# Kernel tuning notes

Measured on AMD Instinct MI355X. Metric: run time of the kernel, lower is better.

Reference implementation:

```python
import jax, jax.numpy as jnp
import numpy as np

ALPHA = 1.702  # GLU sigmoid scale
LIMIT = 7.0    # clamp limit
B, S, H, E, F, TOP_K = 2, 1024, 768, 16, 768, 4


def setup_inputs() -> dict:
    key = jax.random.key(0)
    ks = jax.random.split(key, 7)
    return {
        "hidden_states": jax.random.normal(ks[0], (B, S, H), jnp.float32),
        "router_weight": jax.random.normal(ks[1], (E, H), jnp.float32) * 0.02,
        "router_bias": jax.random.normal(ks[2], (E,), jnp.float32) * 0.02,
        "gate_up_proj": jax.random.normal(ks[3], (E, H, 2 * F), jnp.float32) * 0.02,
        "gate_up_proj_bias": jax.random.normal(ks[4], (E, 2 * F), jnp.float32) * 0.02,
        "down_proj": jax.random.normal(ks[5], (E, F, H), jnp.float32) * 0.02,
        "down_proj_bias": jax.random.normal(ks[6], (E, H), jnp.float32) * 0.02,
        "top_k": TOP_K,
    }


def reference(hidden_states, router_weight, router_bias, gate_up_proj,
              gate_up_proj_bias, down_proj, down_proj_bias, top_k):
    b, s, h = hidden_states.shape
    x = hidden_states.reshape(-1, h)                      # [T, H]
    t = x.shape[0]
    # ---- TopK router ----
    logits = x @ router_weight.T + router_bias            # [T, E]
    top_val, top_idx = jax.lax.top_k(logits, top_k)       # [T, K]
    top_val = jax.nn.softmax(top_val, axis=-1)
    router_scores = jnp.zeros_like(logits).at[
        jnp.arange(t)[:, None], top_idx].set(top_val)     # [T, E]
    # ---- Dense (all-expert) FFN, as in the reference repeat+bmm ----
    gate_up = jnp.einsum('th,ehf->etf', x, gate_up_proj) \
        + gate_up_proj_bias[:, None, :]                   # [E, T, 2F]
    gate = jnp.minimum(gate_up[..., 0::2], LIMIT)         # clamp(max=limit)
    up = jnp.clip(gate_up[..., 1::2], -LIMIT, LIMIT)
    glu = gate * jax.nn.sigmoid(gate * ALPHA)
    expert_out = jnp.einsum('etf,efh->eth', (up + 1.0) * glu, down_proj) \
        + down_proj_bias[:, None, :]                      # [E, T, H]
    expert_out = expert_out.reshape(-1, b, s, h)          # [E, B, S, H]
    w = router_scores.T.reshape(-1, b, s)[..., None]      # [E, B, S, 1]
    routed_out = (expert_out * w).sum(axis=0)             # [B, S, H]
    return routed_out, router_scores
```

## Files before the change

kernel.cpp:

```cpp
#include <hip/hip_runtime.h>
#include <hip/hip_bf16.h>

#define T_TOK 2048
#define H_DIM 768
#define E_NUM 16
#define F_DIM 768
#define TWOF 1536
#define TOPK 4
#define NASSIGN 8192
#define BM 128
#define BK 64
#define KT 12
#define NTILE 80
#define NSLOTP (NTILE * BM)
#define MAXT1 10
#define CHUNK (BM * BK)
#define WTILE (64 * BK)
#define NRTR 256

typedef __bf16 bf16x8 __attribute__((ext_vector_type(8)));
typedef unsigned short us8 __attribute__((ext_vector_type(8)));
typedef float f32x4 __attribute__((ext_vector_type(4)));

__device__ __forceinline__ unsigned short f2bf(float f) {
  unsigned u = __float_as_uint(f);
  u += 0x7FFF + ((u >> 16) & 1);
  return (unsigned short)(u >> 16);
}

__device__ __forceinline__ void gl_lds16(const unsigned short* g, unsigned short* l) {
  __builtin_amdgcn_global_load_lds(
      (const __attribute__((address_space(1))) unsigned int*)g,
      (__attribute__((address_space(3))) unsigned int*)l, 16, 0, 0);
}

__global__ __launch_bounds__(256)
void router_kernel(const float* __restrict__ x, const float* __restrict__ rw,
                   const float* __restrict__ rb, float* __restrict__ scores,
                   int* __restrict__ tk_idx, float* __restrict__ tk_w,
                   int* __restrict__ tmap, float* __restrict__ wgrp) {
  __shared__ float lg[8][16], sc[8][16];
  const int bid = blockIdx.x;
  const int tid = threadIdx.x;
  const int t0 = bid * 8;
  if (tid < 40) {
    tmap[bid * 40 + tid] = 0;
    wgrp[bid * 40 + tid] = 0.0f;
  }
  const int lane32 = tid & 31, tok = tid >> 5;
  const int e = lane32 & 15, q2 = lane32 >> 4;
  const int t = t0 + tok;
  const float* xr = x + (size_t)t * H_DIM + q2 * 384;
  const float* wr = rw + (size_t)e * H_DIM + q2 * 384;
  double a0 = 0, a1 = 0, a2 = 0, a3 = 0;
  #pragma unroll 4
  for (int h = 0; h < 384; h += 4) {
    const f32x4 xv = *(const f32x4*)(xr + h);
    const f32x4 wv = *(const f32x4*)(wr + h);
    a0 += (double)xv[0] * (double)wv[0];
    a1 += (double)xv[1] * (double)wv[1];
    a2 += (double)xv[2] * (double)wv[2];
    a3 += (double)xv[3] * (double)wv[3];
  }
  double acc = (a0 + a1) + (a2 + a3);
  acc += __shfl_xor(acc, 16, 64);
  if (q2 == 0) lg[tok][e] = (float)acc + rb[e];
  __syncthreads();
  if (lane32 == 0) {
    float v[16];
    #pragma unroll
    for (int i = 0; i < 16; ++i) { v[i] = lg[tok][i]; sc[tok][i] = 0.0f; }
    int idx[TOPK]; float val[TOPK];
    for (int k = 0; k < TOPK; ++k) {
      float best = -3.4e38f; int bi = 0;
      for (int i = 0; i < 16; ++i)
        if (v[i] > best) { best = v[i]; bi = i; }
      idx[k] = bi; val[k] = best; v[bi] = -3.4e38f;
    }
    float s = 0.0f, ev[TOPK];
    for (int k = 0; k < TOPK; ++k) { ev[k] = expf(val[k] - val[0]); s += ev[k]; }
    for (int k = 0; k < TOPK; ++k) {
      float wgt = ev[k] / s;
      sc[tok][idx[k]] = wgt;
      tk_idx[t * TOPK + k] = idx[k];
      tk_w[t * TOPK + k] = wgt;
    }
  }
  __syncthreads();
  if (tid < 128)
    scores[(size_t)(t0 + (tid >> 4)) * 16 + (tid & 15)] = sc[tid >> 4][tid & 15];
}

__global__ __launch_bounds__(256)
void group_kernel(const int* __restrict__ tk_idx, const float* __restrict__ tk_w,
                  int* __restrict__ counts, int* __restrict__ offs,
                  int* __restrict__ tmap, float* __restrict__ wgrp) {
  __shared__ int hist[256][16];
  __shared__ int seg[16][16];
  __shared__ int cnt[16], eoff[16];
  const int tid = threadIdx.x;
  int loc[16];
  #pragma unroll
  for (int e = 0; e < 16; ++e) loc[e] = 0;
  const int base = tid * 32;
  int eid[32];
  for (int i = 0; i < 32; ++i) { int e = tk_idx[base + i]; eid[i] = e; loc[e]++; }
  #pragma unroll
  for (int e = 0; e < 16; ++e) hist[tid][e] = loc[e];
  __syncthreads();
  const int s = tid >> 4, e16 = tid & 15;
  {
    int sum = 0;
    #pragma unroll
    for (int j = 0; j < 16; ++j) sum += hist[s * 16 + j][e16];
    seg[s][e16] = sum;
  }
  __syncthreads();
  if (tid < 16) {
    int run = 0;
    #pragma unroll
    for (int s2 = 0; s2 < 16; ++s2) { int t = seg[s2][tid]; seg[s2][tid] = run; run += t; }
    cnt[tid] = run;
  }
  __syncthreads();
  {
    int run = seg[s][e16];
    #pragma unroll
    for (int j = 0; j < 16; ++j) { int t = hist[s * 16 + j][e16]; hist[s * 16 + j][e16] = run; run += t; }
  }
  __syncthreads();
  if (tid == 0) {
    int acc = 0;
    for (int e = 0; e < 16; ++e) { eoff[e] = acc; acc += (cnt[e] + BM - 1) / BM * BM; }
  }
  __syncthreads();
  if (tid < 16) { counts[tid] = cnt[tid]; offs[tid] = eoff[tid]; }
  int run[16];
  #pragma unroll
  for (int e = 0; e < 16; ++e) run[e] = hist[tid][e];
  for (int i = 0; i < 32; ++i) {
    int e = eid[i];
    int slot = eoff[e] + run[e]++;
    tmap[slot] = base + i;
    wgrp[slot] = tk_w[base + i];
  }
}

__global__ __launch_bounds__(512)
void convert_w_kernel(const float* __restrict__ gup, const float* __restrict__ dwn,
                      unsigned short* __restrict__ gw, unsigned short* __restrict__ uw,
                      unsigned short* __restrict__ dw) {
  const int ft = blockIdx.x, kt = blockIdx.y, z = blockIdx.z;
  const int tid = threadIdx.x;
  const int n = tid & 63, k8 = tid >> 6;
  const int doff = n * BK + 8 * (k8 ^ (n & 7));
  __shared__ unsigned short tg[WTILE], tu[WTILE];
  if (z < 16) {
    const int e = z;
    const float* src = gup + ((size_t)(e * H_DIM + kt * 64 + k8 * 8)) * TWOF
                           + 2 * (ft * 64 + n);
    us8 g, u;
    #pragma unroll
    for (int j = 0; j < 8; ++j) {
      const float2 p = *(const float2*)(src + (size_t)j * TWOF);
      g[j] = f2bf(p.x); u[j] = f2bf(p.y);
    }
    *(us8*)&tg[doff] = g;
    *(us8*)&tu[doff] = u;
    __syncthreads();
    const size_t tb = (((size_t)e * KT + kt) * 12 + ft) * WTILE;
    *(us8*)&gw[tb + tid * 8] = *(const us8*)&tg[tid * 8];
    *(us8*)&uw[tb + tid * 8] = *(const us8*)&tu[tid * 8];
  } else {
    const int e = z - 16;
    const float* src = dwn + ((size_t)(e * F_DIM + kt * 64 + k8 * 8)) * H_DIM
                           + ft * 64 + n;
    us8 o;
    #pragma unroll
    for (int j = 0; j < 8; ++j) o[j] = f2bf(src[(size_t)j * H_DIM]);
    *(us8*)&tg[doff] = o;
    __syncthreads();
    const size_t tb = (((size_t)e * KT + kt) * 12 + ft) * WTILE;
    *(us8*)&dw[tb + tid * 8] = *(const us8*)&tg[tid * 8];
  }
}

__global__ __launch_bounds__(256)
void convert_x_kernel(const float* __restrict__ x, const int* __restrict__ tmap,
                      unsigned short* __restrict__ xg) {
  const int tile = blockIdx.x;
  const int kt = blockIdx.y;
  const int tid = threadIdx.x;
  const int r = tid >> 1;
  const int c0 = (tid & 1) * 32;
  const int tok = tmap[tile * BM + r] >> 2;
  const float* src = x + (size_t)tok * H_DIM + kt * 64 + c0;
  unsigned short* dst = xg + ((size_t)tile * KT + kt) * CHUNK + r * BK;
  #pragma unroll
  for (int qq = 0; qq < 4; ++qq) {
    f32x4 a = *(const f32x4*)(src + 8 * qq);
    f32x4 b = *(const f32x4*)(src + 8 * qq + 4);
    us8 o;
    #pragma unroll
    for (int j = 0; j < 4; ++j) { o[j] = f2bf(a[j]); o[4+j] = f2bf(b[j]); }
    const int k8 = (c0 >> 3) + qq;
    *(us8*)&dst[8 * (k8 ^ (r & 7))] = o;
  }
}

__global__ __launch_bounds__(512)
void gemm1_kernel(const unsigned short* __restrict__ xg, const unsigned short* __restrict__ gw,
                  const unsigned short* __restrict__ uw, const float* __restrict__ gupb,
                  const int* __restrict__ counts, const int* __restrict__ offs,
                  unsigned short* __restrict__ act) {
  const int bid = blockIdx.x;
  const int swz = (bid & 7) * 120 + (bid >> 3);
  const int ey = swz / 6, ft = swz % 6;
  const int e = ey / MAXT1, tile = ey % MAXT1;
  const int count = counts[e];
  if (tile * BM >= count) return;
  const int tileg = (offs[e] >> 7) + tile;
  const int tid = threadIdx.x;
  const int wv = tid >> 6, lane = tid & 63;
  const int ml = lane & 15, lh = lane >> 4;
  const int wm = wv >> 2, wn = wv & 3;

  __shared__ unsigned short lA[CHUNK];
  __shared__ unsigned short lBg[CHUNK];
  __shared__ unsigned short lBu[CHUNK];

  const unsigned short* ab = xg + (size_t)tileg * KT * CHUNK;
  const unsigned short* gb = gw + ((size_t)e * KT * 12 + ft * 2) * WTILE;
  const unsigned short* ub = uw + ((size_t)e * KT * 12 + ft * 2) * WTILE;

  f32x4 accg[4][2] = {};
  f32x4 accu[4][2] = {};

  for (int kt = 0; kt < KT; ++kt) {
    const unsigned short* as = ab + kt * CHUNK;
    const unsigned short* gs = gb + (size_t)kt * 12 * WTILE;
    const unsigned short* us = ub + (size_t)kt * 12 * WTILE;
    gl_lds16(as + tid * 8, &lA[tid * 8]);
    gl_lds16(as + (512 + tid) * 8, &lA[(512 + tid) * 8]);
    gl_lds16(gs + tid * 8, &lBg[tid * 8]);
    gl_lds16(gs + (512 + tid) * 8, &lBg[(512 + tid) * 8]);
    gl_lds16(us + tid * 8, &lBu[tid * 8]);
    gl_lds16(us + (512 + tid) * 8, &lBu[(512 + tid) * 8]);
    __syncthreads();
    #pragma unroll
    for (int ks = 0; ks < 2; ++ks) {
      const int slot = ks * 4 + lh;
      bf16x8 af[4];
      #pragma unroll
      for (int mf = 0; mf < 4; ++mf) {
        const int ar = wm * 64 + mf * 16 + ml;
        af[mf] = __builtin_bit_cast(bf16x8, *(const us8*)&lA[ar * BK + 8 * (slot ^ (ar & 7))]);
      }
      #pragma unroll
      for (int nf = 0; nf < 2; ++nf) {
        const int br = wn * 32 + nf * 16 + ml;
        const int ba = (br >> 6) * WTILE + (br & 63) * BK + 8 * (slot ^ (br & 7));
        bf16x8 bg = __builtin_bit_cast(bf16x8, *(const us8*)&lBg[ba]);
        bf16x8 bu = __builtin_bit_cast(bf16x8, *(const us8*)&lBu[ba]);
        #pragma unroll
        for (int mf = 0; mf < 4; ++mf) {
          accg[mf][nf] = __builtin_amdgcn_mfma_f32_16x16x32_bf16(af[mf], bg, accg[mf][nf], 0, 0, 0);
          accu[mf][nf] = __builtin_amdgcn_mfma_f32_16x16x32_bf16(af[mf], bu, accu[mf][nf], 0, 0, 0);
        }
      }
    }
    __syncthreads();
  }
  unsigned short* tbuf = (wn & 2) ? lBg : lA;
  #pragma unroll
  for (int mf = 0; mf < 4; ++mf) {
    #pragma unroll
    for (int nf = 0; nf < 2; ++nf) {
      const int fcl = wn * 32 + nf * 16 + ml;
      const int c = fcl & 63;
      const int fc = ft * 128 + fcl;
      const float bgv = gupb[(size_t)e * TWOF + 2 * fc];
      const float buv = gupb[(size_t)e * TWOF + 2 * fc + 1];
      #pragma unroll
      for (int r = 0; r < 4; ++r) {
        const int m = wm * 64 + mf * 16 + lh * 4 + r;
        float g = accg[mf][nf][r] + bgv;
        float u = accu[mf][nf][r] + buv;
        g = fminf(g, 7.0f);
        u = fminf(fmaxf(u, -7.0f), 7.0f);
        const float glu = g / (1.0f + expf(-1.702f * g));
        tbuf[m * BK + 8 * ((c >> 3) ^ (m & 7)) + (c & 7)] = f2bf((u + 1.0f) * glu);
      }
    }
  }
  __syncthreads();
  unsigned short* ob0 = act + ((size_t)tileg * KT + ft * 2) * CHUNK;
  unsigned short* ob1 = ob0 + CHUNK;
  #pragma unroll
  for (int i = 0; i < 2; ++i) {
    *(us8*)&ob0[(i * 512 + tid) * 8] = *(const us8*)&lA[(i * 512 + tid) * 8];
    *(us8*)&ob1[(i * 512 + tid) * 8] = *(const us8*)&lBg[(i * 512 + tid) * 8];
  }
}

__global__ __launch_bounds__(512)
void gemm2_kernel(const unsigned short* __restrict__ act, const unsigned short* __restrict__ dw,
                  const float* __restrict__ dwnb, const int* __restrict__ counts,
                  const int* __restrict__ offs, const int* __restrict__ tmap,
                  const float* __restrict__ wgrp, float* __restrict__ partial) {
  const int bid = blockIdx.x;
  const int swz = (bid & 7) * 120 + (bid >> 3);
  const int ey = swz / 6, ft = swz % 6;
  const int e = ey / MAXT1, tile = ey % MAXT1;
  const int count = counts[e];
  if (tile * BM >= count) return;
  const int off = offs[e];
  const int tileg = (off >> 7) + tile;
  const int tid = threadIdx.x;
  const int wv = tid >> 6, lane = tid & 63;
  const int ml = lane & 15, lh = lane >> 4;
  const int wm = wv >> 2, wn = wv & 3;

  __shared__ unsigned short lA[CHUNK];
  __shared__ unsigned short lB[CHUNK];

  const unsigned short* ab = act + (size_t)tileg * KT * CHUNK;
  const unsigned short* bb = dw + ((size_t)e * KT * 12 + ft * 2) * WTILE;

  f32x4 acc[4][2] = {};

  for (int kt = 0; kt < KT; ++kt) {
    const unsigned short* as = ab + kt * CHUNK;
    const unsigned short* bs = bb + (size_t)kt * 12 * WTILE;
    gl_lds16(as + tid * 8, &lA[tid * 8]);
    gl_lds16(as + (512 + tid) * 8, &lA[(512 + tid) * 8]);
    gl_lds16(bs + tid * 8, &lB[tid * 8]);
    gl_lds16(bs + (512 + tid) * 8, &lB[(512 + tid) * 8]);
    __syncthreads();
    #pragma unroll
    for (int ks = 0; ks < 2; ++ks) {
      const int slot = ks * 4 + lh;
      bf16x8 af[4];
      #pragma unroll
      for (int mf = 0; mf < 4; ++mf) {
        const int ar = wm * 64 + mf * 16 + ml;
        af[mf] = __builtin_bit_cast(bf16x8, *(const us8*)&lA[ar * BK + 8 * (slot ^ (ar & 7))]);
      }
      #pragma unroll
      for (int nf = 0; nf < 2; ++nf) {
        const int br = wn * 32 + nf * 16 + ml;
        const int ba = (br >> 6) * WTILE + (br & 63) * BK + 8 * (slot ^ (br & 7));
        bf16x8 bv = __builtin_bit_cast(bf16x8, *(const us8*)&lB[ba]);
        #pragma unroll
        for (int mf = 0; mf < 4; ++mf)
          acc[mf][nf] = __builtin_amdgcn_mfma_f32_16x16x32_bf16(af[mf], bv, acc[mf][nf], 0, 0, 0);
      }
    }
    __syncthreads();
  }
  #pragma unroll
  for (int mf = 0; mf < 4; ++mf) {
    #pragma unroll
    for (int nf = 0; nf < 2; ++nf) {
      const int hc = ft * 128 + wn * 32 + nf * 16 + ml;
      const float bias = dwnb[(size_t)e * H_DIM + hc];
      #pragma unroll
      for (int r = 0; r < 4; ++r) {
        const int m = tile * BM + wm * 64 + mf * 16 + lh * 4 + r;
        if (m < count) {
          const int slot = off + m;
          partial[(size_t)tmap[slot] * H_DIM + hc] = wgrp[slot] * (acc[mf][nf][r] + bias);
        }
      }
    }
  }
}

__global__ __launch_bounds__(256)
void reduce_kernel(const float* __restrict__ partial, float* __restrict__ out) {
  const int idx = blockIdx.x * 256 + threadIdx.x;
  const int v = idx * 4;
  const int t = v / H_DIM;
  const int h = v - t * H_DIM;
  f32x4 s = {0, 0, 0, 0};
  #pragma unroll
  for (int k = 0; k < 4; ++k) {
    const f32x4 p = *(const f32x4*)&partial[(size_t)(t * 4 + k) * H_DIM + h];
    s += p;
  }
  *(f32x4*)&out[v] = s;
}

extern "C" void kernel_launch(void* const* d_in, const int* in_sizes, int n_in,
                              void* d_out, int out_size, void* d_ws, size_t ws_size,
                              hipStream_t stream) {
  const float* x    = (const float*)d_in[0];
  const float* rw   = (const float*)d_in[1];
  const float* rb   = (const float*)d_in[2];
  const float* gup  = (const float*)d_in[3];
  const float* gupb = (const float*)d_in[4];
  const float* dwn  = (const float*)d_in[5];
  const float* dwnb = (const float*)d_in[6];
  float* out = (float*)d_out;
  float* scores = out + (size_t)T_TOK * H_DIM;

  char* w = (char*)d_ws;
  int*   tk_idx = (int*)w;            w += NASSIGN * 4;
  float* tk_w   = (float*)w;          w += NASSIGN * 4;
  int*   counts = (int*)w;            w += 64;
  int*   offs   = (int*)w;            w += 64;
  int*   tmap   = (int*)w;            w += NSLOTP * 4;
  float* wgrp   = (float*)w;          w += NSLOTP * 4;
  unsigned short* gw = (unsigned short*)w; w += (size_t)E_NUM * KT * 12 * WTILE * 2;
  unsigned short* uw = (unsigned short*)w; w += (size_t)E_NUM * KT * 12 * WTILE * 2;
  unsigned short* dw = (unsigned short*)w; w += (size_t)E_NUM * KT * 12 * WTILE * 2;
  unsigned short* xg = (unsigned short*)w; w += (size_t)NTILE * KT * CHUNK * 2;
  unsigned short* act = (unsigned short*)w; w += (size_t)NTILE * KT * CHUNK * 2;
  float* partial = (float*)w;         w += (size_t)NASSIGN * H_DIM * 4;

  convert_w_kernel<<<dim3(12, 12, 32), 512, 0, stream>>>(gup, dwn, gw, uw, dw);
  router_kernel<<<NRTR, 256, 0, stream>>>(x, rw, rb, scores, tk_idx, tk_w, tmap, wgrp);
  group_kernel<<<1, 256, 0, stream>>>(tk_idx, tk_w, counts, offs, tmap, wgrp);
  convert_x_kernel<<<dim3(NTILE, KT), 256, 0, stream>>>(x, tmap, xg);
  gemm1_kernel<<<6 * E_NUM * MAXT1, 512, 0, stream>>>(
      xg, gw, uw, gupb, counts, offs, act);
  gemm2_kernel<<<6 * E_NUM * MAXT1, 512, 0, stream>>>(
      act, dw, dwnb, counts, offs, tmap, wgrp, partial);
  reduce_kernel<<<(T_TOK * H_DIM / 4) / 256, 256, 0, stream>>>(partial, out);
}
```

Baseline: 128.6 us.

## Fuse token gather and bf16 conversion of activations into gemm1 A-tile load

Removes the separate convert_x kernel and its bf16 gathered buffer; gemm1 now looks up token indices per tile, loads fp32 rows of x directly, converts them with packed bf16 conversion instructions and writes them swizzled into LDS. This drops one launch and the write/read round trip of the gathered activation buffer. In exchange, each of the six N-tile blocks per M-tile re-gathers and converts the same fp32 rows, so x traffic grows. The A load is now a synchronous register path instead of an async global-to-LDS copy, and the conversion rounding may differ slightly from the old f2bf helper.

```diff
diff --git a/kernel.cpp b/kernel.cpp
--- a/kernel.cpp
+++ b/kernel.cpp
@@ -20,12 +20,19 @@
 
 typedef __bf16 bf16x8 __attribute__((ext_vector_type(8)));
 typedef unsigned short us8 __attribute__((ext_vector_type(8)));
+typedef unsigned uint4v __attribute__((ext_vector_type(4)));
 typedef float f32x4 __attribute__((ext_vector_type(4)));
 
 __device__ __forceinline__ unsigned short f2bf(float f) {
   unsigned u = __float_as_uint(f);
   u += 0x7FFF + ((u >> 16) & 1);
   return (unsigned short)(u >> 16);
+}
+
+__device__ __forceinline__ unsigned cvt_pk(float lo, float hi) {
+  unsigned r;
+  asm("v_cvt_pk_bf16_f32 %0, %1, %2" : "=v"(r) : "v"(lo), "v"(hi));
+  return r;
 }
 
 __device__ __forceinline__ void gl_lds16(const unsigned short* g, unsigned short* l) {
@@ -185,34 +192,11 @@
   }
 }
 
-__global__ __launch_bounds__(256)
-void convert_x_kernel(const float* __restrict__ x, const int* __restrict__ tmap,
-                      unsigned short* __restrict__ xg) {
-  const int tile = blockIdx.x;
-  const int kt = blockIdx.y;
-  const int tid = threadIdx.x;
-  const int r = tid >> 1;
-  const int c0 = (tid & 1) * 32;
-  const int tok = tmap[tile * BM + r] >> 2;
-  const float* src = x + (size_t)tok * H_DIM + kt * 64 + c0;
-  unsigned short* dst = xg + ((size_t)tile * KT + kt) * CHUNK + r * BK;
-  #pragma unroll
-  for (int qq = 0; qq < 4; ++qq) {
-    f32x4 a = *(const f32x4*)(src + 8 * qq);
-    f32x4 b = *(const f32x4*)(src + 8 * qq + 4);
-    us8 o;
-    #pragma unroll
-    for (int j = 0; j < 4; ++j) { o[j] = f2bf(a[j]); o[4+j] = f2bf(b[j]); }
-    const int k8 = (c0 >> 3) + qq;
-    *(us8*)&dst[8 * (k8 ^ (r & 7))] = o;
-  }
-}
-
 __global__ __launch_bounds__(512)
-void gemm1_kernel(const unsigned short* __restrict__ xg, const unsigned short* __restrict__ gw,
+void gemm1_kernel(const float* __restrict__ x, const unsigned short* __restrict__ gw,
                   const unsigned short* __restrict__ uw, const float* __restrict__ gupb,
                   const int* __restrict__ counts, const int* __restrict__ offs,
-                  unsigned short* __restrict__ act) {
+                  const int* __restrict__ tmap, unsigned short* __restrict__ act) {
   const int bid = blockIdx.x;
   const int swz = (bid & 7) * 120 + (bid >> 3);
   const int ey = swz / 6, ft = swz % 6;
@@ -228,20 +212,39 @@
   __shared__ unsigned short lA[CHUNK];
   __shared__ unsigned short lBg[CHUNK];
   __shared__ unsigned short lBu[CHUNK];
-
-  const unsigned short* ab = xg + (size_t)tileg * KT * CHUNK;
+  __shared__ int tokl[BM];
+
+  if (tid < BM) tokl[tid] = tmap[tileg * BM + tid] >> 2;
+
   const unsigned short* gb = gw + ((size_t)e * KT * 12 + ft * 2) * WTILE;
   const unsigned short* ub = uw + ((size_t)e * KT * 12 + ft * 2) * WTILE;
 
+  const int an = tid & 63, akq = tid >> 6;
+  const int aswz = 8 * (akq ^ (an & 7));
+
   f32x4 accg[4][2] = {};
   f32x4 accu[4][2] = {};
 
+  __syncthreads();
+
   for (int kt = 0; kt < KT; ++kt) {
-    const unsigned short* as = ab + kt * CHUNK;
     const unsigned short* gs = gb + (size_t)kt * 12 * WTILE;
     const unsigned short* us = ub + (size_t)kt * 12 * WTILE;
-    gl_lds16(as + tid * 8, &lA[tid * 8]);
-    gl_lds16(as + (512 + tid) * 8, &lA[(512 + tid) * 8]);
+    {
+      const float* xs0 = x + (size_t)tokl[an] * H_DIM + kt * 64 + akq * 8;
+      const float* xs1 = x + (size_t)tokl[an + 64] * H_DIM + kt * 64 + akq * 8;
+      const f32x4 a0 = *(const f32x4*)xs0;
+      const f32x4 a1 = *(const f32x4*)(xs0 + 4);
+      const f32x4 b0 = *(const f32x4*)xs1;
+      const f32x4 b1 = *(const f32x4*)(xs1 + 4);
+      uint4v w0, w1;
+      w0[0] = cvt_pk(a0[0], a0[1]); w0[1] = cvt_pk(a0[2], a0[3]);
+      w0[2] = cvt_pk(a1[0], a1[1]); w0[3] = cvt_pk(a1[2], a1[3]);
+      w1[0] = cvt_pk(b0[0], b0[1]); w1[1] = cvt_pk(b0[2], b0[3]);
+      w1[2] = cvt_pk(b1[0], b1[1]); w1[3] = cvt_pk(b1[2], b1[3]);
+      *(uint4v*)&lA[an * BK + aswz] = w0;
+      *(uint4v*)&lA[(an + 64) * BK + aswz] = w1;
+    }
     gl_lds16(gs + tid * 8, &lBg[tid * 8]);
     gl_lds16(gs + (512 + tid) * 8, &lBg[(512 + tid) * 8]);
     gl_lds16(us + tid * 8, &lBu[tid * 8]);
@@ -414,16 +417,14 @@
   unsigned short* gw = (unsigned short*)w; w += (size_t)E_NUM * KT * 12 * WTILE * 2;
   unsigned short* uw = (unsigned short*)w; w += (size_t)E_NUM * KT * 12 * WTILE * 2;
   unsigned short* dw = (unsigned short*)w; w += (size_t)E_NUM * KT * 12 * WTILE * 2;
-  unsigned short* xg = (unsigned short*)w; w += (size_t)NTILE * KT * CHUNK * 2;
   unsigned short* act = (unsigned short*)w; w += (size_t)NTILE * KT * CHUNK * 2;
   float* partial = (float*)w;         w += (size_t)NASSIGN * H_DIM * 4;
 
   convert_w_kernel<<<dim3(12, 12, 32), 512, 0, stream>>>(gup, dwn, gw, uw, dw);
   router_kernel<<<NRTR, 256, 0, stream>>>(x, rw, rb, scores, tk_idx, tk_w, tmap, wgrp);
   group_kernel<<<1, 256, 0, stream>>>(tk_idx, tk_w, counts, offs, tmap, wgrp);
-  convert_x_kernel<<<dim3(NTILE, KT), 256, 0, stream>>>(x, tmap, xg);
   gemm1_kernel<<<6 * E_NUM * MAXT1, 512, 0, stream>>>(
-      xg, gw, uw, gupb, counts, offs, act);
+      x, gw, uw, gupb, counts, offs, tmap, act);
   gemm2_kernel<<<6 * E_NUM * MAXT1, 512, 0, stream>>>(
       act, dw, dwnb, counts, offs, tmap, wgrp, partial);
   reduce_kernel<<<(T_TOK * H_DIM / 4) / 256, 256, 0, stream>>>(partial, out);
```

After: 132.1 us. 1.03x slower.
